# Kernel optimization log

Hardware: AMD Instinct MI355X
Metric: run time of the kernel (lower is better)

The kernel has to match this reference:

```python
import jax, jax.numpy as jnp
import numpy as np

T, B, DX, DZ = 1000, 4096, 8, 4


def setup_inputs() -> dict:
    key = jax.random.key(0)
    k_obs, k_f, k_h = jax.random.split(key, 3)
    observations = jax.random.normal(k_obs, (T, B, DZ), dtype=jnp.float32)
    # Stable transition matrix: damped identity + small perturbation
    F = 0.95 * jnp.eye(DX, dtype=jnp.float32) + 0.01 * jax.random.normal(k_f, (DX, DX), dtype=jnp.float32)
    H = 0.3 * jax.random.normal(k_h, (DZ, DX), dtype=jnp.float32)
    Q = 0.01 * jnp.eye(DX, dtype=jnp.float32)
    R = 0.1 * jnp.eye(DZ, dtype=jnp.float32)
    init_mean = jnp.zeros((B, DX, 1), dtype=jnp.float32)
    init_cov = jnp.broadcast_to(jnp.eye(DX, dtype=jnp.float32), (B, DX, DX)).copy()
    return {"observations": observations, "F": F, "H": H, "Q": Q, "R": R,
            "init_mean": init_mean, "init_cov": init_cov}


def _kalman_filter(observations, F, H, Q, R, init_mean, init_cov):
    Ht = H.T  # (DX, DZ)
    Ft = F.T  # (DX, DX)

    def step(carry, z):
        mean, cov = carry  # (B,DX,1), (B,DX,DX)
        # project: z_k = H x_k + N(0, R)
        proj_mean = H @ mean                      # (B,DZ,1)
        S = H @ cov @ Ht + R                      # (B,DZ,DZ) innovation covariance
        precision = jnp.linalg.inv(S).swapaxes(-2, -1)  # matches covariance.inverse().mT
        # update
        residual = z[..., None] - proj_mean       # (B,DZ,1)
        K = cov @ Ht @ precision                  # (B,DX,DZ) Kalman gain
        up_mean = mean + K @ residual             # (B,DX,1)
        up_cov = cov - K @ H @ cov                # (B,DX,DX)
        # predict
        pr_mean = F @ up_mean
        pr_cov = F @ up_cov @ Ft + Q
        return (pr_mean, pr_cov), (up_mean[..., 0], up_cov)

    _, (all_means, all_covs) = jax.lax.scan(step, (init_mean, init_cov), observations)
    return all_means, all_covs  # (T,B,DX), (T,B,DX,DX)


def reference(observations, F, H, Q, R, init_mean, init_cov):
    return _kalman_filter(observations, F, H, Q, R, init_mean, init_cov)
```

## Files before the change

### kernel.cpp

```cpp
#include <hip/hip_runtime.h>


constexpr int T_  = 1000;
constexpr int B_  = 4096;
constexpr int TF_ = 128;
constexpr int W_  = 250;
constexpr int L_  = 100;
constexpr int C_  = 10;
constexpr int MEANBLKS_ = C_ * B_ / 256;

typedef float f32x4 __attribute__((ext_vector_type(4)));

__device__ __forceinline__ float det3(float a, float b, float c,
                                      float d, float e, float f,
                                      float g, float h, float i) {
    return a * (e * i - f * h) - b * (d * i - f * g) + c * (d * h - e * g);
}

__global__ __launch_bounds__(256) void kalman_all(
    const float* __restrict__ obs,
    const float* __restrict__ Fm,
    const float* __restrict__ Hm,
    const float* __restrict__ Qm,
    const float* __restrict__ Rm,
    const float* __restrict__ im,
    const float* __restrict__ icov,
    float* __restrict__ out)
{
    __shared__ __align__(16) float AuS[TF_ * 64];
    __shared__ __align__(16) float KtS[TF_ * 32];
    __shared__ __align__(16) float covS[64];
    __shared__ __align__(16) float chtS[32];
    __shared__ __align__(16) float chtTS[32];
    __shared__ __align__(16) float sS[16];
    __shared__ __align__(16) float pTS[16];
    __shared__ __align__(16) float kS[32];
    __shared__ __align__(16) float upS[64];
    __shared__ __align__(16) float upTS[64];
    __shared__ __align__(16) float gS[64];

    const int tid = threadIdx.x;
    const bool meanRole = blockIdx.x < MEANBLKS_;
    const int covT  = meanRole ? 0 : (int)blockIdx.x - MEANBLKS_;
    const int steps = meanRole ? TF_ : ((covT < TF_ ? covT : TF_ - 1) + 1);

    if (tid < 64) {
        const int l  = tid;
        const int i8 = l & 7;
        float hrow[8], hrow2[8], frowA[8], frowB[8];
#pragma unroll
        for (int k = 0; k < 8; ++k) {
            hrow[k]  = Hm[(l & 3) * 8 + k];
            hrow2[k] = Hm[((l >> 2) & 3) * 8 + k];
            frowA[k] = Fm[(l >> 3) * 8 + k];
            frowB[k] = Fm[i8 * 8 + k];
        }
        const float qreg = Qm[l];
        const float rreg = Rm[l & 15];
        const float fij  = Fm[l];
        float hf[4];
#pragma unroll
        for (int m = 0; m < 4; ++m) {
            float acc = 0.f;
#pragma unroll
            for (int k = 0; k < 8; ++k) acc += Hm[m * 8 + k] * Fm[k * 8 + (l & 7)];
            hf[m] = acc;
        }
        float covreg = icov[l];
        covS[l] = covreg;

        for (int t = 0; t < steps; ++t) {
            if (l < 32) {
                const int ia = l >> 2, ja = l & 3;
                const float4* cr = (const float4*)(covS + ia * 8);
                float4 c0 = cr[0], c1 = cr[1];
                float v = c0.x*hrow[0] + c0.y*hrow[1] + c0.z*hrow[2] + c0.w*hrow[3]
                        + c1.x*hrow[4] + c1.y*hrow[5] + c1.z*hrow[6] + c1.w*hrow[7];
                chtS[ia * 4 + ja]  = v;
                chtTS[ja * 8 + ia] = v;
            }
            if (l < 16) {
                const int jb = l & 3;
                const float4* ctr = (const float4*)(chtTS + jb * 8);
                float4 c0 = ctr[0], c1 = ctr[1];
                sS[l] = c0.x*hrow2[0] + c0.y*hrow2[1] + c0.z*hrow2[2] + c0.w*hrow2[3]
                      + c1.x*hrow2[4] + c1.y*hrow2[5] + c1.z*hrow2[6] + c1.w*hrow2[7]
                      + rreg;
            }
            if (l < 16) {
                const float4* sr = (const float4*)sS;
                float4 s0 = sr[0], s1 = sr[1], s2 = sr[2], s3 = sr[3];
                float M00 = det3(s1.y, s1.z, s1.w, s2.y, s2.z, s2.w, s3.y, s3.z, s3.w);
                float M01 = det3(s1.x, s1.z, s1.w, s2.x, s2.z, s2.w, s3.x, s3.z, s3.w);
                float M02 = det3(s1.x, s1.y, s1.w, s2.x, s2.y, s2.w, s3.x, s3.y, s3.w);
                float M03 = det3(s1.x, s1.y, s1.z, s2.x, s2.y, s2.z, s3.x, s3.y, s3.z);
                float det = s0.x * M00 - s0.y * M01 + s0.z * M02 - s0.w * M03;
                const int ic_ = l >> 2, jc = l & 3;
                const int r0 = (ic_ == 0) ? 1 : 0, r1 = (ic_ <= 1) ? 2 : 1, r2 = (ic_ <= 2) ? 3 : 2;
                const int c0i = (jc == 0) ? 1 : 0, c1i = (jc <= 1) ? 2 : 1, c2i = (jc <= 2) ? 3 : 2;
                float cof = det3(sS[r0*4 + c0i], sS[r0*4 + c1i], sS[r0*4 + c2i],
                                 sS[r1*4 + c0i], sS[r1*4 + c1i], sS[r1*4 + c2i],
                                 sS[r2*4 + c0i], sS[r2*4 + c1i], sS[r2*4 + c2i]);
                if ((ic_ + jc) & 1) cof = -cof;
                pTS[jc * 4 + ic_] = cof / det;
            }
            if (l < 32) {
                const int id = l >> 2, jd = l & 3;
                float4 a = *(const float4*)(chtS + id * 4);
                float4 p = *(const float4*)(pTS + jd * 4);
                kS[id * 4 + jd] = a.x*p.x + a.y*p.y + a.z*p.z + a.w*p.w;
            }
            {
                const int ie = l >> 3, je = l & 7;
                float4 kr = *(const float4*)(kS + ie * 4);
                float4 ch = *(const float4*)(chtS + je * 4);
                float v = covreg - (kr.x*ch.x + kr.y*ch.y + kr.z*ch.z + kr.w*ch.w);
                upS[l] = v;
                upTS[je * 8 + ie] = v;
                if (meanRole) {
                    AuS[t * 64 + l] = fij - (kr.x*hf[0] + kr.y*hf[1] + kr.z*hf[2] + kr.w*hf[3]);
                    if (l < 32) KtS[t * 32 + l] = kS[l];
                }
            }
            {
                const int jf = l & 7;
                const float4* ur = (const float4*)(upTS + jf * 8);
                float4 u0 = ur[0], u1 = ur[1];
                gS[l] = frowA[0]*u0.x + frowA[1]*u0.y + frowA[2]*u0.z + frowA[3]*u0.w
                      + frowA[4]*u1.x + frowA[5]*u1.y + frowA[6]*u1.z + frowA[7]*u1.w;
            }
            {
                const float4* gr = (const float4*)(gS + (l >> 3) * 8);
                float4 g0 = gr[0], g1 = gr[1];
                covreg = frowB[0]*g0.x + frowB[1]*g0.y + frowB[2]*g0.z + frowB[3]*g0.w
                       + frowB[4]*g1.x + frowB[5]*g1.y + frowB[6]*g1.z + frowB[7]*g1.w
                       + qreg;
                covS[l] = covreg;
            }
        }
    }
    __syncthreads();

    if (!meanRole) {
        const int w = tid >> 6, l = tid & 63;
        const f32x4 c = *(const f32x4*)(upS + (l & 15) * 4);
        float* base = out + (size_t)T_ * B_ * 8 + (size_t)covT * B_ * 64;
        for (int j = 0; j < 16; ++j) {
            float* gbase = base + ((size_t)(w * 16 + j)) * 4096 + l * 4;
#pragma unroll
            for (int ss = 0; ss < 16; ++ss)
                *(f32x4*)(gbase + ss * 256) = c;
        }
        return;
    }

    const int tg    = blockIdx.x * 256 + tid;
    const int chunk = tg >> 12;
    const int b     = tg & 4095;
    const int t0    = chunk * L_;
    const int s0    = (t0 > W_) ? (t0 - W_) : 0;
    const int tend  = t0 + L_;

    float u[8];
#pragma unroll
    for (int i = 0; i < 8; ++i) u[i] = 0.f;

    int s = s0;
    if (s0 == 0) {
        float m0[8];
#pragma unroll
        for (int i = 0; i < 8; ++i) m0[i] = im[(size_t)b * 8 + i];
        f32x4 z0 = *(const f32x4*)(obs + (size_t)b * 4);
        float r[4];
#pragma unroll
        for (int m = 0; m < 4; ++m) {
            float hm = 0.f;
#pragma unroll
            for (int k = 0; k < 8; ++k) hm += Hm[m * 8 + k] * m0[k];
            r[m] = ((const float*)&z0)[m] - hm;
        }
#pragma unroll
        for (int i = 0; i < 8; ++i) {
            f32x4 kr = *(const f32x4*)(KtS + i * 4);
            u[i] = m0[i] + kr.x*r[0] + kr.y*r[1] + kr.z*r[2] + kr.w*r[3];
        }
        if (t0 == 0) {
            float* mb = out + (size_t)b * 8;
            f32x4 lo = {u[0], u[1], u[2], u[3]};
            f32x4 hi = {u[4], u[5], u[6], u[7]};
            *(f32x4*)mb = lo;
            *(f32x4*)(mb + 4) = hi;
        }
        s = 1;
    }

    f32x4 z = *(const f32x4*)(obs + (size_t)s * B_ * 4 + (size_t)b * 4);
    for (int t = s; t < tend; ++t) {
        const int row = (t < TF_) ? t : TF_ - 1;
        const float* Au = AuS + row * 64;
        const float* Kt = KtS + row * 32;
        const int tn = (t + 1 < tend) ? (t + 1) : t;
        const f32x4 zn = *(const f32x4*)(obs + (size_t)tn * B_ * 4 + (size_t)b * 4);
        float un[8];
#pragma unroll
        for (int i = 0; i < 8; ++i) {
            f32x4 a0 = *(const f32x4*)(Au + i * 8);
            f32x4 a1 = *(const f32x4*)(Au + i * 8 + 4);
            f32x4 kr = *(const f32x4*)(Kt + i * 4);
            un[i] = a0.x*u[0] + a0.y*u[1] + a0.z*u[2] + a0.w*u[3]
                  + a1.x*u[4] + a1.y*u[5] + a1.z*u[6] + a1.w*u[7]
                  + kr.x*z.x  + kr.y*z.y  + kr.z*z.z  + kr.w*z.w;
        }
#pragma unroll
        for (int i = 0; i < 8; ++i) u[i] = un[i];
        z = zn;
        if (t >= t0) {
            float* mb = out + (size_t)t * B_ * 8 + (size_t)b * 8;
            f32x4 lo = {u[0], u[1], u[2], u[3]};
            f32x4 hi = {u[4], u[5], u[6], u[7]};
            *(f32x4*)mb = lo;
            *(f32x4*)(mb + 4) = hi;
        }
    }
}

extern "C" void kernel_launch(void* const* d_in, const int* in_sizes, int n_in,
                              void* d_out, int out_size, void* d_ws, size_t ws_size,
                              hipStream_t stream) {
    const float* obs = (const float*)d_in[0];
    const float* F   = (const float*)d_in[1];
    const float* H   = (const float*)d_in[2];
    const float* Q   = (const float*)d_in[3];
    const float* R   = (const float*)d_in[4];
    const float* im  = (const float*)d_in[5];
    const float* ic  = (const float*)d_in[6];
    kalman_all<<<MEANBLKS_ + T_, 256, 0, stream>>>(obs, F, H, Q, R, im, ic,
                                                   (float*)d_out);
}
```

Measured before the change: 1.393 ms.

## Hoist Riccati recursion into a single-block prepass kernel writing gain tables

The covariance/gain recursion, which is independent of the batch, was recomputed serially inside every block. It now runs once in a separate 64-thread kernel that writes Au, K and covariance tables to workspace. The main kernel loads these tables into shared memory or reads covariance rows directly. This removes redundant serial work per block, at the cost of an extra kernel launch and a dependency that serialises the prepass before the main work.

```diff
diff --git a/kernel.cpp b/kernel.cpp
--- a/kernel.cpp
+++ b/kernel.cpp
@@ -17,18 +17,16 @@
     return a * (e * i - f * h) - b * (d * i - f * g) + c * (d * h - e * g);
 }
 
-__global__ __launch_bounds__(256) void kalman_all(
-    const float* __restrict__ obs,
+__global__ __launch_bounds__(64) void riccati_k(
     const float* __restrict__ Fm,
     const float* __restrict__ Hm,
     const float* __restrict__ Qm,
     const float* __restrict__ Rm,
-    const float* __restrict__ im,
     const float* __restrict__ icov,
-    float* __restrict__ out)
+    float* __restrict__ AuTab,
+    float* __restrict__ KtTab,
+    float* __restrict__ covTab)
 {
-    __shared__ __align__(16) float AuS[TF_ * 64];
-    __shared__ __align__(16) float KtS[TF_ * 32];
     __shared__ __align__(16) float covS[64];
     __shared__ __align__(16) float chtS[32];
     __shared__ __align__(16) float chtTS[32];
@@ -39,111 +37,120 @@
     __shared__ __align__(16) float upTS[64];
     __shared__ __align__(16) float gS[64];
 
+    const int l  = threadIdx.x;
+    const int i8 = l & 7;
+    float hrow[8], hrow2[8], frowA[8], frowB[8];
+#pragma unroll
+    for (int k = 0; k < 8; ++k) {
+        hrow[k]  = Hm[(l & 3) * 8 + k];
+        hrow2[k] = Hm[((l >> 2) & 3) * 8 + k];
+        frowA[k] = Fm[(l >> 3) * 8 + k];
+        frowB[k] = Fm[i8 * 8 + k];
+    }
+    const float qreg = Qm[l];
+    const float rreg = Rm[l & 15];
+    const float fij  = Fm[l];
+    float hf[4];
+#pragma unroll
+    for (int m = 0; m < 4; ++m) {
+        float acc = 0.f;
+#pragma unroll
+        for (int k = 0; k < 8; ++k) acc += Hm[m * 8 + k] * Fm[k * 8 + (l & 7)];
+        hf[m] = acc;
+    }
+    float covreg = icov[l];
+    covS[l] = covreg;
+
+    for (int t = 0; t < TF_; ++t) {
+        if (l < 32) {
+            const int ia = l >> 2, ja = l & 3;
+            const float4* cr = (const float4*)(covS + ia * 8);
+            float4 c0 = cr[0], c1 = cr[1];
+            float v = c0.x*hrow[0] + c0.y*hrow[1] + c0.z*hrow[2] + c0.w*hrow[3]
+                    + c1.x*hrow[4] + c1.y*hrow[5] + c1.z*hrow[6] + c1.w*hrow[7];
+            chtS[ia * 4 + ja]  = v;
+            chtTS[ja * 8 + ia] = v;
+        }
+        if (l < 16) {
+            const int jb = l & 3;
+            const float4* ctr = (const float4*)(chtTS + jb * 8);
+            float4 c0 = ctr[0], c1 = ctr[1];
+            sS[l] = c0.x*hrow2[0] + c0.y*hrow2[1] + c0.z*hrow2[2] + c0.w*hrow2[3]
+                  + c1.x*hrow2[4] + c1.y*hrow2[5] + c1.z*hrow2[6] + c1.w*hrow2[7]
+                  + rreg;
+        }
+        if (l < 16) {
+            const float4* sr = (const float4*)sS;
+            float4 s0 = sr[0], s1 = sr[1], s2 = sr[2], s3 = sr[3];
+            float M00 = det3(s1.y, s1.z, s1.w, s2.y, s2.z, s2.w, s3.y, s3.z, s3.w);
+            float M01 = det3(s1.x, s1.z, s1.w, s2.x, s2.z, s2.w, s3.x, s3.z, s3.w);
+            float M02 = det3(s1.x, s1.y, s1.w, s2.x, s2.y, s2.w, s3.x, s3.y, s3.w);
+            float M03 = det3(s1.x, s1.y, s1.z, s2.x, s2.y, s2.z, s3.x, s3.y, s3.z);
+            float det = s0.x * M00 - s0.y * M01 + s0.z * M02 - s0.w * M03;
+            const int ic_ = l >> 2, jc = l & 3;
+            const int r0 = (ic_ == 0) ? 1 : 0, r1 = (ic_ <= 1) ? 2 : 1, r2 = (ic_ <= 2) ? 3 : 2;
+            const int c0i = (jc == 0) ? 1 : 0, c1i = (jc <= 1) ? 2 : 1, c2i = (jc <= 2) ? 3 : 2;
+            float cof = det3(sS[r0*4 + c0i], sS[r0*4 + c1i], sS[r0*4 + c2i],
+                             sS[r1*4 + c0i], sS[r1*4 + c1i], sS[r1*4 + c2i],
+                             sS[r2*4 + c0i], sS[r2*4 + c1i], sS[r2*4 + c2i]);
+            if ((ic_ + jc) & 1) cof = -cof;
+            pTS[jc * 4 + ic_] = cof / det;
+        }
+        if (l < 32) {
+            const int id = l >> 2, jd = l & 3;
+            float4 a = *(const float4*)(chtS + id * 4);
+            float4 p = *(const float4*)(pTS + jd * 4);
+            kS[id * 4 + jd] = a.x*p.x + a.y*p.y + a.z*p.z + a.w*p.w;
+        }
+        {
+            const int ie = l >> 3, je = l & 7;
+            float4 kr = *(const float4*)(kS + ie * 4);
+            float4 ch = *(const float4*)(chtS + je * 4);
+            float v = covreg - (kr.x*ch.x + kr.y*ch.y + kr.z*ch.z + kr.w*ch.w);
+            upS[l] = v;
+            upTS[je * 8 + ie] = v;
+            covTab[t * 64 + l] = v;
+            AuTab[t * 64 + l]  = fij - (kr.x*hf[0] + kr.y*hf[1] + kr.z*hf[2] + kr.w*hf[3]);
+            if (l < 32) KtTab[t * 32 + l] = kS[l];
+        }
+        {
+            const int jf = l & 7;
+            const float4* ur = (const float4*)(upTS + jf * 8);
+            float4 u0 = ur[0], u1 = ur[1];
+            gS[l] = frowA[0]*u0.x + frowA[1]*u0.y + frowA[2]*u0.z + frowA[3]*u0.w
+                  + frowA[4]*u1.x + frowA[5]*u1.y + frowA[6]*u1.z + frowA[7]*u1.w;
+        }
+        {
+            const float4* gr = (const float4*)(gS + (l >> 3) * 8);
+            float4 g0 = gr[0], g1 = gr[1];
+            covreg = frowB[0]*g0.x + frowB[1]*g0.y + frowB[2]*g0.z + frowB[3]*g0.w
+                   + frowB[4]*g1.x + frowB[5]*g1.y + frowB[6]*g1.z + frowB[7]*g1.w
+                   + qreg;
+            covS[l] = covreg;
+        }
+    }
+}
+
+__global__ __launch_bounds__(256) void kalman2(
+    const float* __restrict__ obs,
+    const float* __restrict__ Hm,
+    const float* __restrict__ im,
+    const float* __restrict__ AuTab,
+    const float* __restrict__ KtTab,
+    const float* __restrict__ covTab,
+    float* __restrict__ out)
+{
+    __shared__ __align__(16) float AuS[TF_ * 64];
+    __shared__ __align__(16) float KtS[TF_ * 32];
+
     const int tid = threadIdx.x;
     const bool meanRole = blockIdx.x < MEANBLKS_;
-    const int covT  = meanRole ? 0 : (int)blockIdx.x - MEANBLKS_;
-    const int steps = meanRole ? TF_ : ((covT < TF_ ? covT : TF_ - 1) + 1);
-
-    if (tid < 64) {
-        const int l  = tid;
-        const int i8 = l & 7;
-        float hrow[8], hrow2[8], frowA[8], frowB[8];
-#pragma unroll
-        for (int k = 0; k < 8; ++k) {
-            hrow[k]  = Hm[(l & 3) * 8 + k];
-            hrow2[k] = Hm[((l >> 2) & 3) * 8 + k];
-            frowA[k] = Fm[(l >> 3) * 8 + k];
-            frowB[k] = Fm[i8 * 8 + k];
-        }
-        const float qreg = Qm[l];
-        const float rreg = Rm[l & 15];
-        const float fij  = Fm[l];
-        float hf[4];
-#pragma unroll
-        for (int m = 0; m < 4; ++m) {
-            float acc = 0.f;
-#pragma unroll
-            for (int k = 0; k < 8; ++k) acc += Hm[m * 8 + k] * Fm[k * 8 + (l & 7)];
-            hf[m] = acc;
-        }
-        float covreg = icov[l];
-        covS[l] = covreg;
-
-        for (int t = 0; t < steps; ++t) {
-            if (l < 32) {
-                const int ia = l >> 2, ja = l & 3;
-                const float4* cr = (const float4*)(covS + ia * 8);
-                float4 c0 = cr[0], c1 = cr[1];
-                float v = c0.x*hrow[0] + c0.y*hrow[1] + c0.z*hrow[2] + c0.w*hrow[3]
-                        + c1.x*hrow[4] + c1.y*hrow[5] + c1.z*hrow[6] + c1.w*hrow[7];
-                chtS[ia * 4 + ja]  = v;
-                chtTS[ja * 8 + ia] = v;
-            }
-            if (l < 16) {
-                const int jb = l & 3;
-                const float4* ctr = (const float4*)(chtTS + jb * 8);
-                float4 c0 = ctr[0], c1 = ctr[1];
-                sS[l] = c0.x*hrow2[0] + c0.y*hrow2[1] + c0.z*hrow2[2] + c0.w*hrow2[3]
-                      + c1.x*hrow2[4] + c1.y*hrow2[5] + c1.z*hrow2[6] + c1.w*hrow2[7]
-                      + rreg;
-            }
-            if (l < 16) {
-                const float4* sr = (const float4*)sS;
-                float4 s0 = sr[0], s1 = sr[1], s2 = sr[2], s3 = sr[3];
-                float M00 = det3(s1.y, s1.z, s1.w, s2.y, s2.z, s2.w, s3.y, s3.z, s3.w);
-                float M01 = det3(s1.x, s1.z, s1.w, s2.x, s2.z, s2.w, s3.x, s3.z, s3.w);
-                float M02 = det3(s1.x, s1.y, s1.w, s2.x, s2.y, s2.w, s3.x, s3.y, s3.w);
-                float M03 = det3(s1.x, s1.y, s1.z, s2.x, s2.y, s2.z, s3.x, s3.y, s3.z);
-                float det = s0.x * M00 - s0.y * M01 + s0.z * M02 - s0.w * M03;
-                const int ic_ = l >> 2, jc = l & 3;
-                const int r0 = (ic_ == 0) ? 1 : 0, r1 = (ic_ <= 1) ? 2 : 1, r2 = (ic_ <= 2) ? 3 : 2;
-                const int c0i = (jc == 0) ? 1 : 0, c1i = (jc <= 1) ? 2 : 1, c2i = (jc <= 2) ? 3 : 2;
-                float cof = det3(sS[r0*4 + c0i], sS[r0*4 + c1i], sS[r0*4 + c2i],
-                                 sS[r1*4 + c0i], sS[r1*4 + c1i], sS[r1*4 + c2i],
-                                 sS[r2*4 + c0i], sS[r2*4 + c1i], sS[r2*4 + c2i]);
-                if ((ic_ + jc) & 1) cof = -cof;
-                pTS[jc * 4 + ic_] = cof / det;
-            }
-            if (l < 32) {
-                const int id = l >> 2, jd = l & 3;
-                float4 a = *(const float4*)(chtS + id * 4);
-                float4 p = *(const float4*)(pTS + jd * 4);
-                kS[id * 4 + jd] = a.x*p.x + a.y*p.y + a.z*p.z + a.w*p.w;
-            }
-            {
-                const int ie = l >> 3, je = l & 7;
-                float4 kr = *(const float4*)(kS + ie * 4);
-                float4 ch = *(const float4*)(chtS + je * 4);
-                float v = covreg - (kr.x*ch.x + kr.y*ch.y + kr.z*ch.z + kr.w*ch.w);
-                upS[l] = v;
-                upTS[je * 8 + ie] = v;
-                if (meanRole) {
-                    AuS[t * 64 + l] = fij - (kr.x*hf[0] + kr.y*hf[1] + kr.z*hf[2] + kr.w*hf[3]);
-                    if (l < 32) KtS[t * 32 + l] = kS[l];
-                }
-            }
-            {
-                const int jf = l & 7;
-                const float4* ur = (const float4*)(upTS + jf * 8);
-                float4 u0 = ur[0], u1 = ur[1];
-                gS[l] = frowA[0]*u0.x + frowA[1]*u0.y + frowA[2]*u0.z + frowA[3]*u0.w
-                      + frowA[4]*u1.x + frowA[5]*u1.y + frowA[6]*u1.z + frowA[7]*u1.w;
-            }
-            {
-                const float4* gr = (const float4*)(gS + (l >> 3) * 8);
-                float4 g0 = gr[0], g1 = gr[1];
-                covreg = frowB[0]*g0.x + frowB[1]*g0.y + frowB[2]*g0.z + frowB[3]*g0.w
-                       + frowB[4]*g1.x + frowB[5]*g1.y + frowB[6]*g1.z + frowB[7]*g1.w
-                       + qreg;
-                covS[l] = covreg;
-            }
-        }
-    }
-    __syncthreads();
 
     if (!meanRole) {
+        const int covT = (int)blockIdx.x - MEANBLKS_;
+        const int row  = (covT < TF_) ? covT : TF_ - 1;
         const int w = tid >> 6, l = tid & 63;
-        const f32x4 c = *(const f32x4*)(upS + (l & 15) * 4);
+        const f32x4 c = *(const f32x4*)(covTab + row * 64 + (l & 15) * 4);
         float* base = out + (size_t)T_ * B_ * 8 + (size_t)covT * B_ * 64;
         for (int j = 0; j < 16; ++j) {
             float* gbase = base + ((size_t)(w * 16 + j)) * 4096 + l * 4;
@@ -153,6 +160,16 @@
         }
         return;
     }
+
+    {
+#pragma unroll
+        for (int i = tid * 4; i < TF_ * 64; i += 1024)
+            *(f32x4*)(AuS + i) = *(const f32x4*)(AuTab + i);
+#pragma unroll
+        for (int i = tid * 4; i < TF_ * 32; i += 1024)
+            *(f32x4*)(KtS + i) = *(const f32x4*)(KtTab + i);
+    }
+    __syncthreads();
 
     const int tg    = blockIdx.x * 256 + tid;
     const int chunk = tg >> 12;
@@ -234,6 +251,11 @@
     const float* R   = (const float*)d_in[4];
     const float* im  = (const float*)d_in[5];
     const float* ic  = (const float*)d_in[6];
-    kalman_all<<<MEANBLKS_ + T_, 256, 0, stream>>>(obs, F, H, Q, R, im, ic,
-                                                   (float*)d_out);
-}
+    float* AuTab  = (float*)d_ws;
+    float* KtTab  = AuTab + (size_t)TF_ * 64;
+    float* covTab = KtTab + (size_t)TF_ * 32;
+
+    riccati_k<<<1, 64, 0, stream>>>(F, H, Q, R, ic, AuTab, KtTab, covTab);
+    kalman2<<<MEANBLKS_ + T_, 256, 0, stream>>>(obs, H, im, AuTab, KtTab,
+                                                covTab, (float*)d_out);
+}
```

Measured after the change: 1.401 ms. No clear change (+0.5%).
